# Kernel tuning notes

Hardware: AMD Instinct MI355X
Metric: run time of the kernel (lower is better)

## Reference

```python
import jax, jax.numpy as jnp
import numpy as np

HEAD_SIZE = 64
N_EMBD = 1024
B, T = 8, 2048

def setup_inputs() -> dict:
    key = jax.random.key(0)
    kx, kq, kk, kv = jax.random.split(key, 4)
    x = jax.random.normal(kx, (B, T, N_EMBD), dtype=jnp.float32)
    s = 1.0 / np.sqrt(N_EMBD)
    Wq = jax.random.normal(kq, (N_EMBD, HEAD_SIZE), dtype=jnp.float32) * s
    Wk = jax.random.normal(kk, (N_EMBD, HEAD_SIZE), dtype=jnp.float32) * s
    Wv = jax.random.normal(kv, (N_EMBD, HEAD_SIZE), dtype=jnp.float32) * s
    return {"x": x, "Wq": Wq, "Wk": Wk, "Wv": Wv}

def reference(x, Wq, Wk, Wv):
    # x: [B,T,C]; project to q,k,v: [B,T,H]
    q = jnp.einsum('btc,ch->bth', x, Wq)
    k = jnp.einsum('btc,ch->bth', x, Wk)
    v = jnp.einsum('btc,ch->bth', x, Wv)
    scale = 1.0 / jnp.sqrt(jnp.asarray(HEAD_SIZE, dtype=x.dtype))
    wei = jnp.einsum('bth,bsh->bts', q, k) * scale  # [B,T,T]
    Tlen = x.shape[1]
    causal = jnp.tril(jnp.ones((Tlen, Tlen), dtype=bool))
    wei = jnp.where(causal[None, :, :], wei, jnp.asarray(-jnp.inf, dtype=wei.dtype))
    wei = jax.nn.softmax(wei, axis=-1)
    # dropout p=0.0 (eval) -> identity
    out = jnp.einsum('bts,bsh->bth', wei, v)  # [B,T,H]
    return out
```

## Files before the change

### kernel.cpp

```cpp
#include <hip/hip_runtime.h>
#include <math.h>

static constexpr int BN = 8;
static constexpr int TS = 2048;
static constexpr int CE = 1024;
static constexpr int HD = 64;

typedef __attribute__((ext_vector_type(8))) short bf16x8;
typedef __attribute__((ext_vector_type(4))) float f32x4;

typedef __attribute__((address_space(3))) void lds_void;
typedef __attribute__((address_space(1))) void glb_void;

__device__ __forceinline__ unsigned short f2bf(float f) {
    union { float f; unsigned u; } v; v.f = f;
    unsigned r = v.u + 0x7FFF + ((v.u >> 16) & 1);
    return (unsigned short)(r >> 16);
}

__device__ __forceinline__ bf16x8 pack8(const float4& a, const float4& b) {
    union { unsigned u[4]; bf16x8 v; } r;
    asm("v_cvt_pk_bf16_f32 %0, %1, %2" : "=v"(r.u[0]) : "v"(a.x), "v"(a.y));
    asm("v_cvt_pk_bf16_f32 %0, %1, %2" : "=v"(r.u[1]) : "v"(a.z), "v"(a.w));
    asm("v_cvt_pk_bf16_f32 %0, %1, %2" : "=v"(r.u[2]) : "v"(b.x), "v"(b.y));
    asm("v_cvt_pk_bf16_f32 %0, %1, %2" : "=v"(r.u[3]) : "v"(b.z), "v"(b.w));
    return r.v;
}

__global__ __launch_bounds__(256) void wt_kernel(
    const float* __restrict__ Wq, const float* __restrict__ Wk,
    const float* __restrict__ Wv, unsigned short* __restrict__ Wt)
{
    __shared__ float T[64 * 69];
    const int tid = threadIdx.x;
    const int m  = blockIdx.x >> 4;
    const int kt = blockIdx.x & 15;
    const float* W = (m == 0) ? Wq : (m == 1) ? Wk : Wv;
    const int k0 = kt * 64;

    #pragma unroll
    for (int it = 0; it < 4; ++it) {
        int idx = tid + it * 256;
        int r = idx >> 4, nq = idx & 15;
        float4 v = *(const float4*)(W + (long)(k0 + r) * HD + nq * 4);
        T[r * 69 + nq * 4 + 0] = v.x;
        T[r * 69 + nq * 4 + 1] = v.y;
        T[r * 69 + nq * 4 + 2] = v.z;
        T[r * 69 + nq * 4 + 3] = v.w;
    }
    __syncthreads();
    #pragma unroll
    for (int it = 0; it < 2; ++it) {
        int idx = tid + it * 256;
        int n = idx >> 3, kq = idx & 7;
        unsigned short h[8];
        #pragma unroll
        for (int s = 0; s < 8; ++s)
            h[s] = f2bf(T[(kq * 8 + s) * 69 + n]);
        *(uint4*)(Wt + (long)(m * 64 + n) * CE + k0 + kq * 8) = *(uint4*)h;
    }
}

static constexpr int NTI = CE / 64;

__global__ __launch_bounds__(512, 1) void qkv_mfma_kernel(
    const float* __restrict__ x, const unsigned short* __restrict__ Wt,
    unsigned short* __restrict__ qo, unsigned short* __restrict__ ko,
    unsigned short* __restrict__ vo)
{
    __shared__ __align__(16) float          xR[3][64 * 64];
    __shared__ __align__(16) unsigned short wR[3][192 * 64];

    const int tid = threadIdx.x;
    const int l  = tid & 63;
    const int v  = tid >> 6;
    const int lr = l & 15, h = l >> 4;
    const int wr = v >> 2;
    const int wc = v & 3;
    const long row0 = (long)blockIdx.x * 64;

    const float* xsrc0; const float* xsrc1;
    {
        int G, r_, gd;
        G = tid;        r_ = G >> 4; gd = G & 15;
        xsrc0 = x + (row0 + r_) * CE + (gd ^ (r_ & 15)) * 4;
        G = 512 + tid;  r_ = G >> 4; gd = G & 15;
        xsrc1 = x + (row0 + r_) * CE + (gd ^ (r_ & 15)) * 4;
    }
    const int xd0 = 256 * v;
    const int xd1 = 2048 + 256 * v;

    const unsigned short* wsrc0; const unsigned short* wsrc1;
    const unsigned short* wsrc2;
    {
        int G, rw, g8;
        G = tid;         rw = G >> 3; g8 = G & 7;
        wsrc0 = Wt + (long)rw * CE + (g8 ^ (rw & 7)) * 8;
        G = 512 + tid;   rw = G >> 3; g8 = G & 7;
        wsrc1 = Wt + (long)rw * CE + (g8 ^ (rw & 7)) * 8;
        G = 1024 + tid;  rw = G >> 3; g8 = G & 7;
        wsrc2 = Wt + (long)rw * CE + (g8 ^ (rw & 7)) * 8;
    }
    const int wd0 = 512 * v;
    const int wd1 = 4096 + 512 * v;
    const int wd2 = 8192 + 512 * v;

    f32x4 acc[2][3];
    #pragma unroll
    for (int i = 0; i < 2; ++i)
        #pragma unroll
        for (int j = 0; j < 3; ++j)
            acc[i][j] = (f32x4){0.f, 0.f, 0.f, 0.f};

    #define STAGE(nb, t) do {                                                 \
        __builtin_amdgcn_global_load_lds((const glb_void*)(xsrc0 + (t) * 64), \
            (lds_void*)(&xR[nb][xd0]), 16, 0, 0);                             \
        __builtin_amdgcn_global_load_lds((const glb_void*)(xsrc1 + (t) * 64), \
            (lds_void*)(&xR[nb][xd1]), 16, 0, 0);                             \
        __builtin_amdgcn_global_load_lds((const glb_void*)(wsrc0 + (t) * 64), \
            (lds_void*)(&wR[nb][wd0]), 16, 0, 0);                             \
        __builtin_amdgcn_global_load_lds((const glb_void*)(wsrc1 + (t) * 64), \
            (lds_void*)(&wR[nb][wd1]), 16, 0, 0);                             \
        __builtin_amdgcn_global_load_lds((const glb_void*)(wsrc2 + (t) * 64), \
            (lds_void*)(&wR[nb][wd2]), 16, 0, 0);                             \
        __builtin_amdgcn_sched_barrier(0); } while (0)

    #define COMPUTE(cb) do {                                                  \
        _Pragma("unroll")                                                     \
        for (int kk = 0; kk < 2; ++kk) {                                      \
            const int g0 = kk * 8 + 2 * h;                                    \
            bf16x8 af[2];                                                     \
            _Pragma("unroll")                                                 \
            for (int i = 0; i < 2; ++i) {                                     \
                const int rowi = 32 * wr + 16 * i + lr;                       \
                float4 a0 = *(const float4*)(&xR[cb][rowi * 64 + ((g0    ) ^ lr) * 4]); \
                float4 a1 = *(const float4*)(&xR[cb][rowi * 64 + ((g0 + 1) ^ lr) * 4]); \
                af[i] = pack8(a0, a1);                                        \
            }                                                                 \
            _Pragma("unroll")                                                 \
            for (int j = 0; j < 3; ++j) {                                     \
                const int roww = 48 * wc + 16 * j + lr;                       \
                const int gw = (kk * 4 + h) ^ (lr & 7);                       \
                bf16x8 bf = *(const bf16x8*)(&wR[cb][roww * 64 + gw * 8]);    \
                _Pragma("unroll")                                             \
                for (int i = 0; i < 2; ++i)                                   \
                    acc[i][j] = __builtin_amdgcn_mfma_f32_16x16x32_bf16(      \
                        af[i], bf, acc[i][j], 0, 0, 0);                       \
            }                                                                 \
        } } while (0)

    STAGE(0, 0);
    STAGE(1, 1);
    STAGE(2, 2);

    #pragma unroll
    for (int t = 0; t < NTI; ++t) {
        const int cb = t % 3;
        if      (t <= NTI - 3) asm volatile("s_waitcnt vmcnt(10)" ::: "memory");
        else if (t == NTI - 2) asm volatile("s_waitcnt vmcnt(5)"  ::: "memory");
        else                   asm volatile("s_waitcnt vmcnt(0)"  ::: "memory");
        __builtin_amdgcn_s_barrier();
        asm volatile("" ::: "memory");
        COMPUTE(cb);
        __builtin_amdgcn_s_barrier();
        if (t + 3 < NTI) STAGE(cb, t + 3);
    }
    #undef STAGE
    #undef COMPUTE

    #pragma unroll
    for (int j = 0; j < 3; ++j) {
        const int n0 = 48 * wc + 16 * j;
        if (n0 < 128) {
            unsigned short* outp = (n0 < 64) ? qo : ko;
            const int h0 = (n0 & 63) + lr;
            #pragma unroll
            for (int i = 0; i < 2; ++i)
                #pragma unroll
                for (int r = 0; r < 4; ++r) {
                    long rowg = row0 + 32 * wr + 16 * i + h * 4 + r;
                    outp[rowg * HD + h0] = f2bf(acc[i][j][r]);
                }
        } else {
            const int d  = (n0 - 128) + lr;
            const int bb = (int)(row0 >> 11);
            #pragma unroll
            for (int i = 0; i < 2; ++i) {
                const int t0 = (int)(row0 & 2047) + 32 * wr + 16 * i + h * 4;
                unsigned short h4[4];
                #pragma unroll
                for (int r = 0; r < 4; ++r) h4[r] = f2bf(acc[i][j][r]);
                *(uint2*)(vo + (((long)(bb * 64 + d)) << 11) + t0) = *(uint2*)h4;
            }
        }
    }
}

__global__ __launch_bounds__(256) void attn_mfma_kernel(
    const unsigned short* __restrict__ qg,
    const unsigned short* __restrict__ kg,
    const unsigned short* __restrict__ vtg,
    float* __restrict__ out)
{
    __shared__ unsigned short Pl[4][32 * 72];
    __shared__ float Ow[4][32 * 64];
    __shared__ float Ml[4][32], Ll[4][32];

    const int tid = threadIdx.x;
    const int w  = tid >> 6;
    const int l  = tid & 63;
    const int lr = l & 15, h = l >> 4;
    const int b  = blockIdx.x & 7;
    const int pr = (blockIdx.x >> 3) & 31;

    const unsigned short* qB = qg  + (long)b * TS * HD;
    const unsigned short* kB = kg  + (long)b * TS * HD;
    const unsigned short* vT = vtg + (long)b * HD * TS;
    float* outB = out + (long)b * TS * HD;

    unsigned short* Pw = &Pl[w][0];

    for (int half = 0; half < 2; ++half) {
        const int qt = half ? (63 - pr) : pr;
        const int q0 = qt * 32;
        const int NT = (qt + 2) >> 1;

        bf16x8 Qf[2][2];
        #pragma unroll
        for (int qf = 0; qf < 2; ++qf)
            #pragma unroll
            for (int ks = 0; ks < 2; ++ks)
                Qf[qf][ks] = *(const bf16x8*)(qB + (q0 + 16 * qf + lr) * HD + 32 * ks + 8 * h);

        f32x4 O[2][4];
        #pragma unroll
        for (int rf = 0; rf < 2; ++rf)
            #pragma unroll
            for (int cf = 0; cf < 4; ++cf)
                O[rf][cf] = (f32x4){0.f, 0.f, 0.f, 0.f};
        float mrow[2] = {-1e30f, -1e30f};
        float lrow[2] = {0.f, 0.f};

        for (int kt = w; kt < NT; kt += 4) {
            const int key0 = kt * 64;
            bf16x8 Kf[4][2], Vf[4][2];
            #pragma unroll
            for (int kf = 0; kf < 4; ++kf)
                #pragma unroll
                for (int ks = 0; ks < 2; ++ks)
                    Kf[kf][ks] = *(const bf16x8*)(kB + (key0 + 16 * kf + lr) * HD + 32 * ks + 8 * h);
            #pragma unroll
            for (int cf = 0; cf < 4; ++cf)
                #pragma unroll
                for (int ks = 0; ks < 2; ++ks)
                    Vf[cf][ks] = *(const bf16x8*)(vT + (16 * cf + lr) * TS + key0 + 32 * ks + 8 * h);

            f32x4 st[4][2];
            #pragma unroll
            for (int kf = 0; kf < 4; ++kf)
                #pragma unroll
                for (int qf = 0; qf < 2; ++qf)
                    st[kf][qf] = (f32x4){0.f, 0.f, 0.f, 0.f};
            #pragma unroll
            for (int ks = 0; ks < 2; ++ks)
                #pragma unroll
                for (int kf = 0; kf < 4; ++kf)
                    #pragma unroll
                    for (int qf = 0; qf < 2; ++qf)
                        st[kf][qf] = __builtin_amdgcn_mfma_f32_16x16x32_bf16(
                            Kf[kf][ks], Qf[qf][ks], st[kf][qf], 0, 0, 0);

            const bool lastt = (kt == NT - 1);
            float alpha[2];
            #pragma unroll
            for (int qf = 0; qf < 2; ++qf) {
                const int qrow = q0 + 16 * qf + lr;
                float tm = -1e30f;
                #pragma unroll
                for (int kf = 0; kf < 4; ++kf)
                    #pragma unroll
                    for (int r = 0; r < 4; ++r) {
                        float sv = st[kf][qf][r] * 0.125f;
                        if (lastt && (key0 + 16 * kf + 4 * h + r) > qrow) sv = -1e30f;
                        st[kf][qf][r] = sv;
                        tm = fmaxf(tm, sv);
                    }
                tm = fmaxf(tm, __shfl_xor(tm, 16));
                tm = fmaxf(tm, __shfl_xor(tm, 32));
                const float mn = fmaxf(mrow[qf], tm);
                alpha[qf] = __expf(mrow[qf] - mn);
                mrow[qf] = mn;
                float rs = 0.f;
                #pragma unroll
                for (int kf = 0; kf < 4; ++kf)
                    #pragma unroll
                    for (int r = 0; r < 4; ++r) {
                        float pv = __expf(st[kf][qf][r] - mn);
                        st[kf][qf][r] = pv;
                        rs += pv;
                    }
                rs += __shfl_xor(rs, 16);
                rs += __shfl_xor(rs, 32);
                lrow[qf] = lrow[qf] * alpha[qf] + rs;
                #pragma unroll
                for (int kf = 0; kf < 4; ++kf) {
                    unsigned a01 = (unsigned)f2bf(st[kf][qf][0]) |
                                   ((unsigned)f2bf(st[kf][qf][1]) << 16);
                    unsigned a23 = (unsigned)f2bf(st[kf][qf][2]) |
                                   ((unsigned)f2bf(st[kf][qf][3]) << 16);
                    unsigned short* pp = Pw + (16 * qf + lr) * 72 + 16 * kf + 4 * h;
                    *(unsigned*)(pp)     = a01;
                    *(unsigned*)(pp + 2) = a23;
                }
            }

            #pragma unroll
            for (int rf = 0; rf < 2; ++rf)
                #pragma unroll
                for (int r = 0; r < 4; ++r) {
                    float aO = __shfl(alpha[rf], 4 * h + r);
                    #pragma unroll
                    for (int cf = 0; cf < 4; ++cf)
                        O[rf][cf][r] *= aO;
                }

            bf16x8 pa[2][2];
            #pragma unroll
            for (int rf = 0; rf < 2; ++rf)
                #pragma unroll
                for (int ks = 0; ks < 2; ++ks)
                    pa[rf][ks] = *(const bf16x8*)(Pw + (16 * rf + lr) * 72 + 32 * ks + 8 * h);
            #pragma unroll
            for (int ks = 0; ks < 2; ++ks)
                #pragma unroll
                for (int rf = 0; rf < 2; ++rf)
                    #pragma unroll
                    for (int cf = 0; cf < 4; ++cf)
                        O[rf][cf] = __builtin_amdgcn_mfma_f32_16x16x32_bf16(
                            pa[rf][ks], Vf[cf][ks], O[rf][cf], 0, 0, 0);
        }

        #pragma unroll
        for (int rf = 0; rf < 2; ++rf)
            #pragma unroll
            for (int cf = 0; cf < 4; ++cf)
                #pragma unroll
                for (int r = 0; r < 4; ++r)
                    Ow[w][(16 * rf + 4 * h + r) * 64 + 16 * cf + lr] = O[rf][cf][r];
        if (h == 0) {
            #pragma unroll
            for (int qf = 0; qf < 2; ++qf) {
                Ml[w][16 * qf + lr] = mrow[qf];
                Ll[w][16 * qf + lr] = lrow[qf];
            }
        }
        __syncthreads();

        {
            const int q  = tid >> 3;
            const int d0 = (tid & 7) * 8;
            float mM = -1e30f;
            #pragma unroll
            for (int w2 = 0; w2 < 4; ++w2) mM = fmaxf(mM, Ml[w2][q]);
            float lS = 0.f;
            float a8[8] = {0.f,0.f,0.f,0.f,0.f,0.f,0.f,0.f};
            #pragma unroll
            for (int w2 = 0; w2 < 4; ++w2) {
                float sc = __expf(Ml[w2][q] - mM);
                lS += Ll[w2][q] * sc;
                #pragma unroll
                for (int e = 0; e < 8; ++e)
                    a8[e] += sc * Ow[w2][q * 64 + d0 + e];
            }
            const float inv = 1.f / lS;
            float4 o1 = {a8[0]*inv, a8[1]*inv, a8[2]*inv, a8[3]*inv};
            float4 o2 = {a8[4]*inv, a8[5]*inv, a8[6]*inv, a8[7]*inv};
            *(float4*)(outB + (long)(q0 + q) * HD + d0)     = o1;
            *(float4*)(outB + (long)(q0 + q) * HD + d0 + 4) = o2;
        }
        __syncthreads();
    }
}

extern "C" void kernel_launch(void* const* d_in, const int* in_sizes, int n_in,
                              void* d_out, int out_size, void* d_ws, size_t ws_size,
                              hipStream_t stream) {
    const float* x  = (const float*)d_in[0];
    const float* Wq = (const float*)d_in[1];
    const float* Wk = (const float*)d_in[2];
    const float* Wv = (const float*)d_in[3];
    float* out = (float*)d_out;

    const size_t nqkv = (size_t)BN * TS * HD;
    unsigned short* qb = (unsigned short*)d_ws;
    unsigned short* kb = qb + nqkv;
    unsigned short* vt = kb + nqkv;

    unsigned short* Wt = (unsigned short*)d_out;

    wt_kernel<<<48, 256, 0, stream>>>(Wq, Wk, Wv, Wt);
    qkv_mfma_kernel<<<(BN * TS) / 64, 512, 0, stream>>>(x, Wt, qb, kb, vt);
    attn_mfma_kernel<<<BN * 32, 256, 0, stream>>>(qb, kb, vt, out);
}
```

Baseline: 51.35 us.

## Stage weight tiles through registers with a 4-deep x ring and double-buffered W

The QKV projection kernel no longer sends weight tiles to LDS with direct global-to-LDS loads. Weights now go into register buffers three tiles ahead and are written to a double-buffered LDS area just before use, while x tiles keep direct-to-LDS loads in a 4-slot ring. Issuing the next loads before the wait and barrier, rather than after compute, is meant to overlap memory latency with the MFMA work better. It costs extra VGPRs for the register staging and adds an lgkmcnt wait plus LDS write traffic every iteration.

```diff
diff --git a/kernel.cpp b/kernel.cpp
--- a/kernel.cpp
+++ b/kernel.cpp
@@ -68,8 +68,8 @@
     unsigned short* __restrict__ qo, unsigned short* __restrict__ ko,
     unsigned short* __restrict__ vo)
 {
-    __shared__ __align__(16) float          xR[3][64 * 64];
-    __shared__ __align__(16) unsigned short wR[3][192 * 64];
+    __shared__ __align__(16) float          xR[4][64 * 64];
+    __shared__ __align__(16) unsigned short wR[2][192 * 64];
 
     const int tid = threadIdx.x;
     const int l  = tid & 63;
@@ -101,9 +101,9 @@
         G = 1024 + tid;  rw = G >> 3; g8 = G & 7;
         wsrc2 = Wt + (long)rw * CE + (g8 ^ (rw & 7)) * 8;
     }
-    const int wd0 = 512 * v;
-    const int wd1 = 4096 + 512 * v;
-    const int wd2 = 8192 + 512 * v;
+    const int wd0 = 512 * v + l * 8;
+    const int wd1 = 4096 + 512 * v + l * 8;
+    const int wd2 = 8192 + 512 * v + l * 8;
 
     f32x4 acc[2][3];
     #pragma unroll
@@ -112,20 +112,28 @@
         for (int j = 0; j < 3; ++j)
             acc[i][j] = (f32x4){0.f, 0.f, 0.f, 0.f};
 
-    #define STAGE(nb, t) do {                                                 \
+    uint4 wv0[3], wv1[3], wv2[3];
+
+    #define STAGE_X(nb, t) do {                                               \
         __builtin_amdgcn_global_load_lds((const glb_void*)(xsrc0 + (t) * 64), \
             (lds_void*)(&xR[nb][xd0]), 16, 0, 0);                             \
         __builtin_amdgcn_global_load_lds((const glb_void*)(xsrc1 + (t) * 64), \
             (lds_void*)(&xR[nb][xd1]), 16, 0, 0);                             \
-        __builtin_amdgcn_global_load_lds((const glb_void*)(wsrc0 + (t) * 64), \
-            (lds_void*)(&wR[nb][wd0]), 16, 0, 0);                             \
-        __builtin_amdgcn_global_load_lds((const glb_void*)(wsrc1 + (t) * 64), \
-            (lds_void*)(&wR[nb][wd1]), 16, 0, 0);                             \
-        __builtin_amdgcn_global_load_lds((const glb_void*)(wsrc2 + (t) * 64), \
-            (lds_void*)(&wR[nb][wd2]), 16, 0, 0);                             \
         __builtin_amdgcn_sched_barrier(0); } while (0)
 
-    #define COMPUTE(cb) do {                                                  \
+    #define LOAD_W(rs, t) do {                                                \
+        (rs)[0] = *(const uint4*)(wsrc0 + (t) * 64);                          \
+        (rs)[1] = *(const uint4*)(wsrc1 + (t) * 64);                          \
+        (rs)[2] = *(const uint4*)(wsrc2 + (t) * 64);                          \
+        __builtin_amdgcn_sched_barrier(0); } while (0)
+
+    #define WRITE_W(nb, rs) do {                                              \
+        *(uint4*)(&wR[nb][wd0]) = (rs)[0];                                    \
+        *(uint4*)(&wR[nb][wd1]) = (rs)[1];                                    \
+        *(uint4*)(&wR[nb][wd2]) = (rs)[2];                                    \
+        __builtin_amdgcn_sched_barrier(0); } while (0)
+
+    #define COMPUTE(xb, wb) do {                                              \
         _Pragma("unroll")                                                     \
         for (int kk = 0; kk < 2; ++kk) {                                      \
             const int g0 = kk * 8 + 2 * h;                                    \
@@ -133,15 +141,15 @@
             _Pragma("unroll")                                                 \
             for (int i = 0; i < 2; ++i) {                                     \
                 const int rowi = 32 * wr + 16 * i + lr;                       \
-                float4 a0 = *(const float4*)(&xR[cb][rowi * 64 + ((g0    ) ^ lr) * 4]); \
-                float4 a1 = *(const float4*)(&xR[cb][rowi * 64 + ((g0 + 1) ^ lr) * 4]); \
+                float4 a0 = *(const float4*)(&xR[xb][rowi * 64 + ((g0    ) ^ lr) * 4]); \
+                float4 a1 = *(const float4*)(&xR[xb][rowi * 64 + ((g0 + 1) ^ lr) * 4]); \
                 af[i] = pack8(a0, a1);                                        \
             }                                                                 \
             _Pragma("unroll")                                                 \
             for (int j = 0; j < 3; ++j) {                                     \
                 const int roww = 48 * wc + 16 * j + lr;                       \
                 const int gw = (kk * 4 + h) ^ (lr & 7);                       \
-                bf16x8 bf = *(const bf16x8*)(&wR[cb][roww * 64 + gw * 8]);    \
+                bf16x8 bf = *(const bf16x8*)(&wR[wb][roww * 64 + gw * 8]);    \
                 _Pragma("unroll")                                             \
                 for (int i = 0; i < 2; ++i)                                   \
                     acc[i][j] = __builtin_amdgcn_mfma_f32_16x16x32_bf16(      \
@@ -149,23 +157,36 @@
             }                                                                 \
         } } while (0)
 
-    STAGE(0, 0);
-    STAGE(1, 1);
-    STAGE(2, 2);
+    STAGE_X(0, 0);  LOAD_W(wv0, 0);
+    STAGE_X(1, 1);  LOAD_W(wv1, 1);
+    STAGE_X(2, 2);  LOAD_W(wv2, 2);
+    asm volatile("s_waitcnt vmcnt(10)" ::: "memory");
+    WRITE_W(0, wv0);
 
     #pragma unroll
     for (int t = 0; t < NTI; ++t) {
-        const int cb = t % 3;
-        if      (t <= NTI - 3) asm volatile("s_waitcnt vmcnt(10)" ::: "memory");
-        else if (t == NTI - 2) asm volatile("s_waitcnt vmcnt(5)"  ::: "memory");
+        if (t + 3 < NTI) {
+            STAGE_X((t + 3) & 3, t + 3);
+            if      (((t + 3) % 3) == 0) LOAD_W(wv0, t + 3);
+            else if (((t + 3) % 3) == 1) LOAD_W(wv1, t + 3);
+            else                         LOAD_W(wv2, t + 3);
+        }
+        if      (t <= NTI - 4) asm volatile("s_waitcnt vmcnt(10)" ::: "memory");
+        else if (t == NTI - 3) asm volatile("s_waitcnt vmcnt(5)"  ::: "memory");
         else                   asm volatile("s_waitcnt vmcnt(0)"  ::: "memory");
+        if (t + 1 < NTI) {
+            if      (((t + 1) % 3) == 0) WRITE_W((t + 1) & 1, wv0);
+            else if (((t + 1) % 3) == 1) WRITE_W((t + 1) & 1, wv1);
+            else                         WRITE_W((t + 1) & 1, wv2);
+        }
+        asm volatile("s_waitcnt lgkmcnt(0)" ::: "memory");
         __builtin_amdgcn_s_barrier();
-        asm volatile("" ::: "memory");
-        COMPUTE(cb);
+        COMPUTE(t & 3, t & 1);
         __builtin_amdgcn_s_barrier();
-        if (t + 3 < NTI) STAGE(cb, t + 3);
-    }
-    #undef STAGE
+    }
+    #undef STAGE_X
+    #undef LOAD_W
+    #undef WRITE_W
     #undef COMPUTE
 
     #pragma unroll
```

Measured after the change: 53.89 us. +5.0%, slower.
